# Performance work log

Measured on AMD Instinct MI355X. Metric: run time of the kernel, lower is better.

## Reference

```python
import jax, jax.numpy as jnp
import numpy as np

B, T, C, H = 2, 2048, 1024, 16
D = C // H  # head_dim = 64

def setup_inputs() -> dict:
    key = jax.random.key(0)
    ks = jax.random.split(key, 9)
    s = 1.0 / np.sqrt(C)
    return {
        "x": jax.random.normal(ks[0], (B, T, C), dtype=jnp.float32),
        "Wq": jax.random.uniform(ks[1], (C, C), jnp.float32, -s, s),
        "bq": jax.random.uniform(ks[2], (C,), jnp.float32, -s, s),
        "Wk": jax.random.uniform(ks[3], (C, C), jnp.float32, -s, s),
        "bk": jax.random.uniform(ks[4], (C,), jnp.float32, -s, s),
        "Wv": jax.random.uniform(ks[5], (C, C), jnp.float32, -s, s),
        "bv": jax.random.uniform(ks[6], (C,), jnp.float32, -s, s),
        "Wp": jax.random.uniform(ks[7], (C, C), jnp.float32, -s, s),
        "bp": jax.random.uniform(ks[8], (C,), jnp.float32, -s, s),
    }

def reference(x, Wq, bq, Wk, bk, Wv, bv, Wp, bp):
    # Linear layers: torch nn.Linear weight is [out,in], so x @ W.T + b
    q = x @ Wq.T + bq
    k = x @ Wk.T + bk
    v = x @ Wv.T + bv
    # [B,T,C] -> [B,H,T,D]
    q = q.reshape(B, T, H, D).transpose(0, 2, 1, 3)
    k = k.reshape(B, T, H, D).transpose(0, 2, 1, 3)
    v = v.reshape(B, T, H, D).transpose(0, 2, 1, 3)
    att = jnp.einsum("bhqd,bhkd->bhqk", q, k) / jnp.sqrt(jnp.float32(D))
    causal = jnp.tril(jnp.ones((T, T), dtype=bool))  # [T,T]
    att = jnp.where(causal, att, jnp.float32(-jnp.inf))
    att = jax.nn.softmax(att, axis=-1)
    out = jnp.einsum("bhqk,bhkd->bhqd", att, v)
    out = out.transpose(0, 2, 1, 3).reshape(B, T, C)
    return out @ Wp.T + bp
```

## Files before the change

kernel.cpp:

```cpp
#include <hip/hip_runtime.h>
#include <hip/hip_bf16.h>

typedef __bf16 bf16x8 __attribute__((ext_vector_type(8)));
typedef __bf16 bf16x4 __attribute__((ext_vector_type(4)));
typedef __bf16 bf16x2 __attribute__((ext_vector_type(2)));
typedef float  f32x4  __attribute__((ext_vector_type(4)));
typedef float  f32x16v __attribute__((ext_vector_type(16)));

#define MFMA16(A,B,Cc) __builtin_amdgcn_mfma_f32_16x16x32_bf16(A,B,Cc,0,0,0)
#define MFMA32(A,B,Cc) __builtin_amdgcn_mfma_f32_32x32x16_bf16(A,B,Cc,0,0,0)

__device__ inline unsigned pack2(float a, float b) {
  union { bf16x2 v; unsigned u; } t;
  t.v[0] = (__bf16)a; t.v[1] = (__bf16)b;
  return t.u;
}
__device__ inline bf16x8 frag4(unsigned w0, unsigned w1, unsigned w2, unsigned w3) {
  union { unsigned u[4]; bf16x8 v; } t;
  t.u[0] = w0; t.u[1] = w1; t.u[2] = w2; t.u[3] = w3;
  return t.v;
}

__device__ inline void pswap(unsigned& a, unsigned& b) {
#if __has_builtin(__builtin_amdgcn_permlane32_swap)
  auto r = __builtin_amdgcn_permlane32_swap(a, b, false, false);
  a = r[0]; b = r[1];
#else
  asm volatile("v_permlane32_swap_b32 %0, %1" : "+v"(a), "+v"(b));
#endif
}
__device__ inline float cross32_max(float v) {
  unsigned a = __builtin_bit_cast(unsigned, v), b = a;
  pswap(a, b);
  return fmaxf(__builtin_bit_cast(float, a), __builtin_bit_cast(float, b));
}
__device__ inline float cross32_sum(float v) {
  unsigned a = __builtin_bit_cast(unsigned, v), b = a;
  pswap(a, b);
  return __builtin_bit_cast(float, a) + __builtin_bit_cast(float, b);
}

__global__ __launch_bounds__(256) void conv_kernel(
    const float* __restrict__ x,
    const float* __restrict__ Wq, const float* __restrict__ Wk,
    const float* __restrict__ Wv, const float* __restrict__ Wp,
    __bf16* __restrict__ xb, __bf16* __restrict__ Wb)
{
  const int z = blockIdx.y;
  const float* src;
  __bf16* dst;
  int n4;
  if (z == 0) { src = x;  dst = xb; n4 = 1048576; }
  else {
    src = (z == 1) ? Wq : (z == 2) ? Wk : (z == 3) ? Wv : Wp;
    dst = Wb + (size_t)(z - 1) * 1048576;
    n4  = 262144;
  }
  const f32x4* s4 = (const f32x4*)src;
  for (int i = blockIdx.x * 256 + threadIdx.x; i < n4; i += gridDim.x * 256) {
    const f32x4 v = s4[i];
    bf16x4 o;
#pragma unroll
    for (int j = 0; j < 4; ++j) o[j] = (__bf16)v[j];
    *(bf16x4*)(dst + (size_t)i * 4) = o;
  }
}

__device__ inline void gemm_core(const __bf16* __restrict__ A,
                                 const __bf16* __restrict__ W,
                                 int m0, int n0,
                                 __bf16* As, __bf16* Bs,
                                 f32x4 (&acc)[4][4])
{
  const int tid = threadIdx.x, lane = tid & 63;
  const int wid = tid >> 6, wr = wid >> 1, wc = wid & 1;
  const int g = lane >> 4, cl = lane & 15;
  const int sr = tid >> 2, sk = (tid & 3) * 8;

  for (int k0 = 0; k0 < 1024; k0 += 32) {
    bf16x8 a0 = *(const bf16x8*)(A + (size_t)(m0 + sr)      * 1024 + k0 + sk);
    bf16x8 a1 = *(const bf16x8*)(A + (size_t)(m0 + sr + 64) * 1024 + k0 + sk);
    bf16x8 b0 = *(const bf16x8*)(W + (size_t)(n0 + sr)      * 1024 + k0 + sk);
    bf16x8 b1 = *(const bf16x8*)(W + (size_t)(n0 + sr + 64) * 1024 + k0 + sk);
    __syncthreads();
    *(bf16x8*)(As + sr * 32 + sk)        = a0;
    *(bf16x8*)(As + (sr + 64) * 32 + sk) = a1;
    *(bf16x8*)(Bs + sr * 32 + sk)        = b0;
    *(bf16x8*)(Bs + (sr + 64) * 32 + sk) = b1;
    __syncthreads();
    bf16x8 af[4], bfr[4];
#pragma unroll
    for (int m = 0; m < 4; ++m)
      af[m] = *(const bf16x8*)(As + (wr * 64 + m * 16 + cl) * 32 + g * 8);
#pragma unroll
    for (int n = 0; n < 4; ++n)
      bfr[n] = *(const bf16x8*)(Bs + (wc * 64 + n * 16 + cl) * 32 + g * 8);
#pragma unroll
    for (int m = 0; m < 4; ++m)
#pragma unroll
      for (int n = 0; n < 4; ++n)
        acc[m][n] = MFMA16(af[m], bfr[n], acc[m][n]);
  }
}

__global__ __launch_bounds__(256) void gemm_qkv128(
    const __bf16* __restrict__ xb, const __bf16* __restrict__ Wb,
    const float* __restrict__ bq, const float* __restrict__ bk,
    const float* __restrict__ bv,
    __bf16* __restrict__ Qw, __bf16* __restrict__ Kw, __bf16* __restrict__ Vw)
{
  __shared__ __align__(16) __bf16 As[128 * 32];
  __shared__ __align__(16) __bf16 Bs[128 * 32];

  const int orig = blockIdx.x;
  const int wg   = (orig & 7) * 96 + (orig >> 3);
  const int z    = wg >> 8;
  const int rem  = wg & 255;
  const int m0   = (rem >> 3) * 128;
  const int n0   = (rem & 7) * 128;

  const __bf16* W  = Wb + (size_t)z * 1048576;
  const float*  bi = (z == 0) ? bq : (z == 1) ? bk : bv;
  __bf16*       out = (z == 0) ? Qw : (z == 1) ? Kw : Vw;

  f32x4 acc[4][4] = {};
  gemm_core(xb, W, m0, n0, As, Bs, acc);

  const int lane = threadIdx.x & 63, wid = threadIdx.x >> 6;
  const int wr = wid >> 1, wc = wid & 1;
  const int g = lane >> 4, cl = lane & 15;

  float bvv[4];
#pragma unroll
  for (int n = 0; n < 4; ++n) bvv[n] = bi[n0 + wc * 64 + n * 16 + cl];

#pragma unroll
  for (int m = 0; m < 4; ++m)
#pragma unroll
    for (int n = 0; n < 4; ++n) {
      const int col = n0 + wc * 64 + n * 16 + cl;
      const int h = col >> 6, d = col & 63;
      if (z == 2) {
        const int row0 = m0 + wr * 64 + m * 16 + g * 4;
        const int b2 = row0 >> 11, t0 = row0 & 2047;
        bf16x4 v4;
#pragma unroll
        for (int j = 0; j < 4; ++j) v4[j] = (__bf16)(acc[m][n][j] + bvv[n]);
        *(bf16x4*)(out + (size_t)(b2 * 16 + h) * 131072 + (size_t)d * 2048 + t0) = v4;
      } else {
#pragma unroll
        for (int j = 0; j < 4; ++j) {
          const int row = m0 + wr * 64 + m * 16 + g * 4 + j;
          const int b2 = row >> 11, t = row & 2047;
          out[(size_t)(b2 * 16 + h) * 131072 + (size_t)t * 64 + d] =
              (__bf16)(acc[m][n][j] + bvv[n]);
        }
      }
    }
}

__global__ __launch_bounds__(256) void gemm_proj128(
    const __bf16* __restrict__ A, const __bf16* __restrict__ W,
    const float* __restrict__ bi, float* __restrict__ outp)
{
  __shared__ __align__(16) __bf16 As[128 * 32];
  __shared__ __align__(16) __bf16 Bs[128 * 32];

  const int orig = blockIdx.x;
  const int wg   = (orig & 7) * 32 + (orig >> 3);
  const int m0   = (wg >> 3) * 128;
  const int n0   = (wg & 7) * 128;

  f32x4 acc[4][4] = {};
  gemm_core(A, W, m0, n0, As, Bs, acc);

  const int lane = threadIdx.x & 63, wid = threadIdx.x >> 6;
  const int wr = wid >> 1, wc = wid & 1;
  const int g = lane >> 4, cl = lane & 15;

  float bvv[4];
#pragma unroll
  for (int n = 0; n < 4; ++n) bvv[n] = bi[n0 + wc * 64 + n * 16 + cl];
#pragma unroll
  for (int m = 0; m < 4; ++m)
#pragma unroll
    for (int n = 0; n < 4; ++n) {
      const int col = n0 + wc * 64 + n * 16 + cl;
#pragma unroll
      for (int j = 0; j < 4; ++j) {
        const int row = m0 + wr * 64 + m * 16 + g * 4 + j;
        outp[(size_t)row * 1024 + col] = acc[m][n][j] + bvv[n];
      }
    }
}

__global__ __launch_bounds__(256, 4) void attn_kernel(
    const __bf16* __restrict__ Q, const __bf16* __restrict__ K,
    const __bf16* __restrict__ Vt, __bf16* __restrict__ Oc)
{
  const int bh  = blockIdx.x;
  const int p   = blockIdx.y;
  const int w   = threadIdx.x >> 6;
  const int lane = threadIdx.x & 63;
  const int l31 = lane & 31, hi = lane >> 5;
  const float SC = 0.18033688f;
  const float DT = 16.6f;

  const __bf16* Qb = Q  + (size_t)bh * 131072;
  const __bf16* Kb = K  + (size_t)bh * 131072;
  const __bf16* Vb = Vt + (size_t)bh * 131072;
  const __bf16* vrow0 = Vb + (size_t)l31 * 2048;
  const __bf16* vrow1 = Vb + (size_t)(32 + l31) * 2048;

  __shared__ __bf16 SO[8][64][34];
  __shared__ float  SML[8][64][2];

  const int qsS[2] = { p * 32, (63 - p) * 32 };
  const int nS[2]  = { p + 1, 64 - p };

#pragma unroll
  for (int ph = 0; ph < 2; ++ph) {
    const int qs = qsS[ph], nT = nS[ph];
    bf16x8 qf[4];
#pragma unroll
    for (int c = 0; c < 4; ++c)
      qf[c] = *(const bf16x8*)(Qb + (qs + l31) * 64 + c * 16 + hi * 8);

    f32x16v o0 = {}, o1 = {};
    float M = -1e30f, L = 0.f;
    float MS = M * SC;

    bf16x8 kf[4];
#pragma unroll
    for (int c = 0; c < 4; ++c)
      kf[c] = *(const bf16x8*)(Kb + (w * 32 + l31) * 64 + c * 16 + hi * 8);

    for (int t = w; t < nT; t += 4) {
      const int kv0 = t * 32;
      const int tn = t + 4;
      bf16x8 kn[4];
      const bool hasNext = tn < nT;
      if (hasNext) {
#pragma unroll
        for (int c = 0; c < 4; ++c)
          kn[c] = *(const bf16x8*)(Kb + (tn * 32 + l31) * 64 + c * 16 + hi * 8);
      }

      f32x16v sA = {}, sB = {};
      sA = MFMA32(kf[0], qf[0], sA);
      sB = MFMA32(kf[1], qf[1], sB);
      sA = MFMA32(kf[2], qf[2], sA);
      sB = MFMA32(kf[3], qf[3], sB);
      f32x16v s = sA + sB;

      if (t == nT - 1) {
#pragma unroll
        for (int r = 0; r < 16; ++r) {
          const int kl = (r & 3) + 8 * (r >> 2) + 4 * hi;
          if (kl > l31) s[r] = -1e30f;
        }
      }
      float mt = fmaxf(s[0], s[1]);
#pragma unroll
      for (int r = 2; r < 16; ++r) mt = fmaxf(mt, s[r]);
      mt = cross32_max(mt);
      if (!__all(mt <= M + DT)) {
        const float Mn = fmaxf(M, mt);
        const float rs = exp2f((M - Mn) * SC);
        o0 *= rs; o1 *= rs; L *= rs; M = Mn; MS = M * SC;
      }
      float pr[16];
      float lt = 0.f;
#pragma unroll
      for (int r = 0; r < 16; ++r) {
        pr[r] = exp2f(__builtin_fmaf(s[r], SC, -MS));
        lt += pr[r];
      }
      L += cross32_sum(lt);

      unsigned c0 = pack2(pr[0],  pr[1]),  c1 = pack2(pr[2],  pr[3]);
      unsigned c2 = pack2(pr[4],  pr[5]),  c3 = pack2(pr[6],  pr[7]);
      unsigned c4 = pack2(pr[8],  pr[9]),  c5 = pack2(pr[10], pr[11]);
      unsigned c6 = pack2(pr[12], pr[13]), c7 = pack2(pr[14], pr[15]);
      pswap(c0, c2);
      pswap(c1, c3);
      pswap(c4, c6);
      pswap(c5, c7);
      const bf16x8 pf0 = frag4(c0, c1, c2, c3);
      const bf16x8 pf1 = frag4(c4, c5, c6, c7);

      bf16x8 va;
      va = *(const bf16x8*)(vrow0 + kv0 + hi * 8);       o0 = MFMA32(va, pf0, o0);
      va = *(const bf16x8*)(vrow1 + kv0 + hi * 8);       o1 = MFMA32(va, pf0, o1);
      va = *(const bf16x8*)(vrow0 + kv0 + 16 + hi * 8);  o0 = MFMA32(va, pf1, o0);
      va = *(const bf16x8*)(vrow1 + kv0 + 16 + hi * 8);  o1 = MFMA32(va, pf1, o1);

      if (hasNext) {
#pragma unroll
        for (int c = 0; c < 4; ++c) kf[c] = kn[c];
      }
    }

    const int slot = ph * 4 + w;
#pragma unroll
    for (int q4 = 0; q4 < 4; ++q4) {
      bf16x4 a, b;
#pragma unroll
      for (int j = 0; j < 4; ++j) {
        a[j] = (__bf16)o0[q4 * 4 + j];
        b[j] = (__bf16)o1[q4 * 4 + j];
      }
      *(bf16x4*)&SO[slot][lane][q4 * 4]      = a;
      *(bf16x4*)&SO[slot][lane][16 + q4 * 4] = b;
    }
    SML[slot][lane][0] = M;
    SML[slot][lane][1] = L;
  }

  __syncthreads();
  if (w < 2) {
    const int base = w * 4;
    const int qs = qsS[w];
    float Mw[4], Lw[4];
#pragma unroll
    for (int s = 0; s < 4; ++s) {
      Mw[s] = SML[base + s][lane][0];
      Lw[s] = SML[base + s][lane][1];
    }
    const float Ms = fmaxf(fmaxf(Mw[0], Mw[1]), fmaxf(Mw[2], Mw[3]));
    float r[4], Lt = 0.f;
#pragma unroll
    for (int s = 0; s < 4; ++s) {
      r[s] = exp2f((Mw[s] - Ms) * SC);
      Lt += Lw[s] * r[s];
    }
    const float inv = 1.0f / Lt;

    const int b = bh >> 4, h = bh & 15;
    const int tq = qs + l31;
    __bf16* orow = Oc + (size_t)(b * 2048 + tq) * 1024 + h * 64;
#pragma unroll
    for (int q4 = 0; q4 < 4; ++q4) {
      bf16x4 v0, v1;
      float acc0[4] = {}, acc1[4] = {};
#pragma unroll
      for (int s = 0; s < 4; ++s) {
        const bf16x4 a4 = *(const bf16x4*)&SO[base + s][lane][q4 * 4];
        const bf16x4 b4 = *(const bf16x4*)&SO[base + s][lane][16 + q4 * 4];
#pragma unroll
        for (int j = 0; j < 4; ++j) {
          acc0[j] += (float)a4[j] * r[s];
          acc1[j] += (float)b4[j] * r[s];
        }
      }
#pragma unroll
      for (int j = 0; j < 4; ++j) {
        v0[j] = (__bf16)(acc0[j] * inv);
        v1[j] = (__bf16)(acc1[j] * inv);
      }
      const int d0 = 8 * q4 + 4 * hi;
      *(bf16x4*)(orow + d0)      = v0;
      *(bf16x4*)(orow + 32 + d0) = v1;
    }
  }
}

extern "C" void kernel_launch(void* const* d_in, const int* in_sizes, int n_in,
                              void* d_out, int out_size, void* d_ws, size_t ws_size,
                              hipStream_t stream) {
  const float* x  = (const float*)d_in[0];
  const float* Wq = (const float*)d_in[1];
  const float* bq = (const float*)d_in[2];
  const float* Wk = (const float*)d_in[3];
  const float* bk = (const float*)d_in[4];
  const float* Wv = (const float*)d_in[5];
  const float* bv = (const float*)d_in[6];
  const float* Wp = (const float*)d_in[7];
  const float* bp = (const float*)d_in[8];

  __bf16* Qw  = (__bf16*)d_ws;
  __bf16* Kw  = Qw + (size_t)4194304;
  __bf16* Vw  = Kw + (size_t)4194304;
  __bf16* xbA = Vw + (size_t)4194304;
  __bf16* Wb  = xbA + (size_t)4194304;

  conv_kernel<<<dim3(512, 5), 256, 0, stream>>>(x, Wq, Wk, Wv, Wp, xbA, Wb);
  gemm_qkv128<<<768, 256, 0, stream>>>(xbA, Wb, bq, bk, bv, Qw, Kw, Vw);
  attn_kernel<<<dim3(32, 32), 256, 0, stream>>>(Qw, Kw, Vw, xbA );
  gemm_proj128<<<256, 256, 0, stream>>>(xbA , Wb + (size_t)3 * 1048576,
                                        bp, (float*)d_out);
}
```

Before: 150.7 us.

## Use direct global-to-LDS loads in GEMM and restructure attention tile loop

```diff
diff --git a/kernel.cpp b/kernel.cpp
--- a/kernel.cpp
+++ b/kernel.cpp
@@ -1,5 +1,6 @@
 #include <hip/hip_runtime.h>
 #include <hip/hip_bf16.h>
+#include <stdint.h>
 
 typedef __bf16 bf16x8 __attribute__((ext_vector_type(8)));
 typedef __bf16 bf16x4 __attribute__((ext_vector_type(4)));
@@ -38,6 +39,12 @@
   unsigned a = __builtin_bit_cast(unsigned, v), b = a;
   pswap(a, b);
   return __builtin_bit_cast(float, a) + __builtin_bit_cast(float, b);
+}
+
+__device__ inline void gl16(const __bf16* g, __bf16* l) {
+  __builtin_amdgcn_global_load_lds(
+      (const __attribute__((address_space(1))) void*)(uintptr_t)g,
+      (__attribute__((address_space(3))) void*)(uintptr_t)l, 16, 0, 0);
 }
 
 __global__ __launch_bounds__(256) void conv_kernel(
@@ -76,17 +83,15 @@
   const int wid = tid >> 6, wr = wid >> 1, wc = wid & 1;
   const int g = lane >> 4, cl = lane & 15;
   const int sr = tid >> 2, sk = (tid & 3) * 8;
+  __bf16* AsW = As + (tid & 192) * 8;
+  __bf16* BsW = Bs + (tid & 192) * 8;
 
   for (int k0 = 0; k0 < 1024; k0 += 32) {
-    bf16x8 a0 = *(const bf16x8*)(A + (size_t)(m0 + sr)      * 1024 + k0 + sk);
-    bf16x8 a1 = *(const bf16x8*)(A + (size_t)(m0 + sr + 64) * 1024 + k0 + sk);
-    bf16x8 b0 = *(const bf16x8*)(W + (size_t)(n0 + sr)      * 1024 + k0 + sk);
-    bf16x8 b1 = *(const bf16x8*)(W + (size_t)(n0 + sr + 64) * 1024 + k0 + sk);
     __syncthreads();
-    *(bf16x8*)(As + sr * 32 + sk)        = a0;
-    *(bf16x8*)(As + (sr + 64) * 32 + sk) = a1;
-    *(bf16x8*)(Bs + sr * 32 + sk)        = b0;
-    *(bf16x8*)(Bs + (sr + 64) * 32 + sk) = b1;
+    gl16(A + (size_t)(m0 + sr)      * 1024 + k0 + sk, AsW);
+    gl16(A + (size_t)(m0 + sr + 64) * 1024 + k0 + sk, AsW + 2048);
+    gl16(W + (size_t)(n0 + sr)      * 1024 + k0 + sk, BsW);
+    gl16(W + (size_t)(n0 + sr + 64) * 1024 + k0 + sk, BsW + 2048);
     __syncthreads();
     bf16x8 af[4], bfr[4];
 #pragma unroll
@@ -194,6 +199,72 @@
     }
 }
 
+__device__ inline void attn_tile(
+    const __bf16* __restrict__ Kb, const __bf16* __restrict__ vrow0,
+    const __bf16* __restrict__ vrow1, const bf16x8 (&qf)[4],
+    int kv0, bool diag, int l31, int hi,
+    float& M, float& MS, float& L, f32x16v& o0, f32x16v& o1)
+{
+  const float SC = 0.18033688f;
+  const float DT = 16.6f;
+
+  const bf16x8 kf0 = *(const bf16x8*)(Kb + (kv0 + l31) * 64 +      hi * 8);
+  const bf16x8 kf1 = *(const bf16x8*)(Kb + (kv0 + l31) * 64 + 16 + hi * 8);
+  const bf16x8 kf2 = *(const bf16x8*)(Kb + (kv0 + l31) * 64 + 32 + hi * 8);
+  const bf16x8 kf3 = *(const bf16x8*)(Kb + (kv0 + l31) * 64 + 48 + hi * 8);
+  const bf16x8 va0 = *(const bf16x8*)(vrow0 + kv0 + hi * 8);
+  const bf16x8 va1 = *(const bf16x8*)(vrow1 + kv0 + hi * 8);
+  const bf16x8 va2 = *(const bf16x8*)(vrow0 + kv0 + 16 + hi * 8);
+  const bf16x8 va3 = *(const bf16x8*)(vrow1 + kv0 + 16 + hi * 8);
+
+  f32x16v s = {};
+  s = MFMA32(kf0, qf[0], s);
+  s = MFMA32(kf1, qf[1], s);
+  s = MFMA32(kf2, qf[2], s);
+  s = MFMA32(kf3, qf[3], s);
+
+  if (diag) {
+#pragma unroll
+    for (int r = 0; r < 16; ++r) {
+      const int kl = (r & 3) + 8 * (r >> 2) + 4 * hi;
+      if (kl > l31) s[r] = -1e30f;
+    }
+  }
+  float mt = fmaxf(s[0], s[1]);
+#pragma unroll
+  for (int r = 2; r < 16; ++r) mt = fmaxf(mt, s[r]);
+  mt = cross32_max(mt);
+  if (!__all(mt <= M + DT)) {
+    const float Mn = fmaxf(M, mt);
+    const float rs = exp2f((M - Mn) * SC);
+    o0 *= rs; o1 *= rs; L *= rs; M = Mn; MS = M * SC;
+  }
+  float pr[16];
+  float lt = 0.f;
+#pragma unroll
+  for (int r = 0; r < 16; ++r) {
+    pr[r] = exp2f(__builtin_fmaf(s[r], SC, -MS));
+    lt += pr[r];
+  }
+  L += cross32_sum(lt);
+
+  unsigned c0 = pack2(pr[0],  pr[1]),  c1 = pack2(pr[2],  pr[3]);
+  unsigned c2 = pack2(pr[4],  pr[5]),  c3 = pack2(pr[6],  pr[7]);
+  unsigned c4 = pack2(pr[8],  pr[9]),  c5 = pack2(pr[10], pr[11]);
+  unsigned c6 = pack2(pr[12], pr[13]), c7 = pack2(pr[14], pr[15]);
+  pswap(c0, c2);
+  pswap(c1, c3);
+  pswap(c4, c6);
+  pswap(c5, c7);
+  const bf16x8 pf0 = frag4(c0, c1, c2, c3);
+  const bf16x8 pf1 = frag4(c4, c5, c6, c7);
+
+  o0 = MFMA32(va0, pf0, o0);
+  o1 = MFMA32(va1, pf0, o1);
+  o0 = MFMA32(va2, pf1, o0);
+  o1 = MFMA32(va3, pf1, o1);
+}
+
 __global__ __launch_bounds__(256, 4) void attn_kernel(
     const __bf16* __restrict__ Q, const __bf16* __restrict__ K,
     const __bf16* __restrict__ Vt, __bf16* __restrict__ Oc)
@@ -204,7 +275,6 @@
   const int lane = threadIdx.x & 63;
   const int l31 = lane & 31, hi = lane >> 5;
   const float SC = 0.18033688f;
-  const float DT = 16.6f;
 
   const __bf16* Qb = Q  + (size_t)bh * 131072;
   const __bf16* Kb = K  + (size_t)bh * 131072;
@@ -212,7 +282,7 @@
   const __bf16* vrow0 = Vb + (size_t)l31 * 2048;
   const __bf16* vrow1 = Vb + (size_t)(32 + l31) * 2048;
 
-  __shared__ __bf16 SO[8][64][34];
+  __shared__ __bf16 SO[8][64][36];
   __shared__ float  SML[8][64][2];
 
   const int qsS[2] = { p * 32, (63 - p) * 32 };
@@ -230,76 +300,9 @@
     float M = -1e30f, L = 0.f;
     float MS = M * SC;
 
-    bf16x8 kf[4];
-#pragma unroll
-    for (int c = 0; c < 4; ++c)
-      kf[c] = *(const bf16x8*)(Kb + (w * 32 + l31) * 64 + c * 16 + hi * 8);
-
-    for (int t = w; t < nT; t += 4) {
-      const int kv0 = t * 32;
-      const int tn = t + 4;
-      bf16x8 kn[4];
-      const bool hasNext = tn < nT;
-      if (hasNext) {
-#pragma unroll
-        for (int c = 0; c < 4; ++c)
-          kn[c] = *(const bf16x8*)(Kb + (tn * 32 + l31) * 64 + c * 16 + hi * 8);
-      }
-
-      f32x16v sA = {}, sB = {};
-      sA = MFMA32(kf[0], qf[0], sA);
-      sB = MFMA32(kf[1], qf[1], sB);
-      sA = MFMA32(kf[2], qf[2], sA);
-      sB = MFMA32(kf[3], qf[3], sB);
-      f32x16v s = sA + sB;
-
-      if (t == nT - 1) {
-#pragma unroll
-        for (int r = 0; r < 16; ++r) {
-          const int kl = (r & 3) + 8 * (r >> 2) + 4 * hi;
-          if (kl > l31) s[r] = -1e30f;
-        }
-      }
-      float mt = fmaxf(s[0], s[1]);
-#pragma unroll
-      for (int r = 2; r < 16; ++r) mt = fmaxf(mt, s[r]);
-      mt = cross32_max(mt);
-      if (!__all(mt <= M + DT)) {
-        const float Mn = fmaxf(M, mt);
-        const float rs = exp2f((M - Mn) * SC);
-        o0 *= rs; o1 *= rs; L *= rs; M = Mn; MS = M * SC;
-      }
-      float pr[16];
-      float lt = 0.f;
-#pragma unroll
-      for (int r = 0; r < 16; ++r) {
-        pr[r] = exp2f(__builtin_fmaf(s[r], SC, -MS));
-        lt += pr[r];
-      }
-      L += cross32_sum(lt);
-
-      unsigned c0 = pack2(pr[0],  pr[1]),  c1 = pack2(pr[2],  pr[3]);
-      unsigned c2 = pack2(pr[4],  pr[5]),  c3 = pack2(pr[6],  pr[7]);
-      unsigned c4 = pack2(pr[8],  pr[9]),  c5 = pack2(pr[10], pr[11]);
-      unsigned c6 = pack2(pr[12], pr[13]), c7 = pack2(pr[14], pr[15]);
-      pswap(c0, c2);
-      pswap(c1, c3);
-      pswap(c4, c6);
-      pswap(c5, c7);
-      const bf16x8 pf0 = frag4(c0, c1, c2, c3);
-      const bf16x8 pf1 = frag4(c4, c5, c6, c7);
-
-      bf16x8 va;
-      va = *(const bf16x8*)(vrow0 + kv0 + hi * 8);       o0 = MFMA32(va, pf0, o0);
-      va = *(const bf16x8*)(vrow1 + kv0 + hi * 8);       o1 = MFMA32(va, pf0, o1);
-      va = *(const bf16x8*)(vrow0 + kv0 + 16 + hi * 8);  o0 = MFMA32(va, pf1, o0);
-      va = *(const bf16x8*)(vrow1 + kv0 + 16 + hi * 8);  o1 = MFMA32(va, pf1, o1);
-
-      if (hasNext) {
-#pragma unroll
-        for (int c = 0; c < 4; ++c) kf[c] = kn[c];
-      }
-    }
+    for (int t = w; t < nT; t += 4)
+      attn_tile(Kb, vrow0, vrow1, qf, t * 32, t == nT - 1, l31, hi,
+                M, MS, L, o0, o1);
 
     const int slot = ph * 4 + w;
 #pragma unroll
```

New measurement: 134.3 us. 1.12x faster.
